# Performance work log

Measured on AMD Instinct MI355X. Metric: run time of the kernel, lower is better.

Reference implementation:

```python
import jax, jax.numpy as jnp
import numpy as np
from jax import lax

RADIUS = 2

def make_kernels(radius):
    # Faithfully reproduces the torch __init__, INCLUDING the bug where
    # NE is computed from the already-normalized NW and SE from SW.
    r = radius
    k = 2 * r + 1
    w = np.ones((k, k), dtype=np.float32)
    L = w.copy(); L[:, r + 1:] = 0
    R = w.copy(); R[:, :r] = 0
    U = w.copy(); U[r + 1:, :] = 0
    D = w.copy(); D[:r, :] = 0
    NW, NE, SW, SE = U.copy(), U.copy(), D.copy(), D.copy()
    half = (r + 1) * k
    L = L / half; R = R / half; U = U / half; D = D / half
    NW[:, r + 1:] = 0
    NE[:, :r] = 0
    SW[:, r + 1:] = 0
    SE[:, :r] = 0
    NW = NW / (r + 1) ** 2
    NE = NW / (r + 1) ** 2  # bug in original: uses new NW
    SW = SW / (r + 1) ** 2
    SE = SW / (r + 1) ** 2  # bug in original: uses new SW
    # order matches d channels 0..7 in forward: L,R,U,D,NW,NE,SW,SE
    return jnp.asarray(np.stack([L, R, U, D, NW, NE, SW, SE])[:, None])  # [8,1,k,k]

def setup_inputs() -> dict:
    key = jax.random.key(0)
    x = jax.random.uniform(key, (8, 3, 768, 768), dtype=jnp.float32)
    return {"x": x, "kernels": make_kernels(RADIUS), "iteration": 3}

def reference(x, kernels, iteration):
    B, C, H, W = x.shape
    k = kernels.shape[-1]
    r = (k - 1) // 2
    # fuse the per-channel loop: treat each (image, channel) as its own sample
    xc = x.reshape(B * C, 1, H, W)

    def step(xc, _):
        # all 8 directional box filters in one conv: [BC,8,H,W]
        conv = lax.conv_general_dilated(
            xc, kernels, window_strides=(1, 1), padding=[(r, r), (r, r)],
            dimension_numbers=("NCHW", "OIHW", "NCHW"))
        d = conv - xc                                   # [BC,8,H,W]
        idx = jnp.argmin(jnp.abs(d), axis=1, keepdims=True)
        dm = jnp.take_along_axis(d, idx, axis=1)        # [BC,1,H,W]
        return xc + dm, None

    xc, _ = lax.scan(step, xc, None, length=iteration)
    return xc.reshape(B, C, H, W)
```

## Files before the change

kernel.cpp:

```cpp
#include <hip/hip_runtime.h>
#include <math.h>


typedef float f4v __attribute__((ext_vector_type(4)));
typedef float f2v __attribute__((ext_vector_type(2), aligned(8)));

#define TW 64
#define TH 32

template<int H2, int W2, bool LAST>
__device__ __forceinline__ void step(const float* __restrict__ X,
                                     float* __restrict__ Y,
                                     float* __restrict__ outp,
                                     int gy0, int gx0, int tid) {
    constexpr int PW = W2 + 4;
    constexpr int SC = W2 / 4;
    constexpr int NSEG = H2 * SC;
    const float w15 = 1.0f / 15.0f;
    const float w9  = 1.0f / 9.0f;
    const float w81 = (1.0f / 9.0f) / 9.0f;

    const bool interior = (gy0 >= 0) && (gx0 >= 0) &&
                          (gy0 + H2 <= 768) && (gx0 + W2 <= 768);

    for (int s = tid; s < NSEG; s += 256) {
        const int y  = s / SC;
        const int xs = (s - y * SC) * 4;
        const float* rp = X + y * PW + xs;

        float acc[8][4];
        #pragma unroll
        for (int d = 0; d < 8; d++)
            #pragma unroll
            for (int j = 0; j < 4; j++) acc[d][j] = 0.0f;
        float ctr[4];

        #pragma unroll
        for (int r = 0; r < 5; r++) {
            const float* p = rp + r * PW;
            f4v lo = *(const f4v*)p;
            f4v hi = *(const f4v*)(p + 4);
            float w[8] = {lo.x, lo.y, lo.z, lo.w, hi.x, hi.y, hi.z, hi.w};

            #pragma unroll
            for (int j = 0; j < 4; j++) {
                acc[0][j] = fmaf(w15, w[j + 0], acc[0][j]);
                acc[0][j] = fmaf(w15, w[j + 1], acc[0][j]);
                acc[0][j] = fmaf(w15, w[j + 2], acc[0][j]);
                acc[1][j] = fmaf(w15, w[j + 2], acc[1][j]);
                acc[1][j] = fmaf(w15, w[j + 3], acc[1][j]);
                acc[1][j] = fmaf(w15, w[j + 4], acc[1][j]);
                if (r < 3) {
                    acc[2][j] = fmaf(w15, w[j + 0], acc[2][j]);
                    acc[2][j] = fmaf(w15, w[j + 1], acc[2][j]);
                    acc[2][j] = fmaf(w15, w[j + 2], acc[2][j]);
                    acc[2][j] = fmaf(w15, w[j + 3], acc[2][j]);
                    acc[2][j] = fmaf(w15, w[j + 4], acc[2][j]);
                    acc[4][j] = fmaf(w9,  w[j + 0], acc[4][j]);
                    acc[4][j] = fmaf(w9,  w[j + 1], acc[4][j]);
                    acc[4][j] = fmaf(w9,  w[j + 2], acc[4][j]);
                    acc[5][j] = fmaf(w81, w[j + 0], acc[5][j]);
                    acc[5][j] = fmaf(w81, w[j + 1], acc[5][j]);
                    acc[5][j] = fmaf(w81, w[j + 2], acc[5][j]);
                }
                if (r >= 2) {
                    acc[3][j] = fmaf(w15, w[j + 0], acc[3][j]);
                    acc[3][j] = fmaf(w15, w[j + 1], acc[3][j]);
                    acc[3][j] = fmaf(w15, w[j + 2], acc[3][j]);
                    acc[3][j] = fmaf(w15, w[j + 3], acc[3][j]);
                    acc[3][j] = fmaf(w15, w[j + 4], acc[3][j]);
                    acc[6][j] = fmaf(w9,  w[j + 0], acc[6][j]);
                    acc[6][j] = fmaf(w9,  w[j + 1], acc[6][j]);
                    acc[6][j] = fmaf(w9,  w[j + 2], acc[6][j]);
                    acc[7][j] = fmaf(w81, w[j + 0], acc[7][j]);
                    acc[7][j] = fmaf(w81, w[j + 1], acc[7][j]);
                    acc[7][j] = fmaf(w81, w[j + 2], acc[7][j]);
                }
                if (r == 2) ctr[j] = w[j + 2];
            }
        }

        f4v R;
        #pragma unroll
        for (int j = 0; j < 4; j++) {
            const float c = ctr[j];
            const float e0 = acc[0][j] - c, e1 = acc[1][j] - c;
            const float e2 = acc[2][j] - c, e3 = acc[3][j] - c;
            const float e4 = acc[4][j] - c, e5 = acc[5][j] - c;
            const float e6 = acc[6][j] - c, e7 = acc[7][j] - c;
            float m01 = (fabsf(e1) < fabsf(e0)) ? e1 : e0;
            float m23 = (fabsf(e3) < fabsf(e2)) ? e3 : e2;
            float m45 = (fabsf(e5) < fabsf(e4)) ? e5 : e4;
            float m67 = (fabsf(e7) < fabsf(e6)) ? e7 : e6;
            float mA  = (fabsf(m23) < fabsf(m01)) ? m23 : m01;
            float mB  = (fabsf(m67) < fabsf(m45)) ? m67 : m45;
            float bd  = (fabsf(mB)  < fabsf(mA))  ? mB  : mA;
            const float res = c + bd;
            if (j == 0) R.x = res; else if (j == 1) R.y = res;
            else if (j == 2) R.z = res; else R.w = res;
        }

        if (LAST) {
            *(f4v*)(outp + y * 768 + xs) = R;
        } else if (interior) {
            *(f4v*)(Y + y * W2 + xs) = R;
        } else {
            const bool rowin = ((unsigned)(gy0 + y) < 768u);
            R.x = (rowin && (unsigned)(gx0 + xs + 0) < 768u) ? R.x : 0.0f;
            R.y = (rowin && (unsigned)(gx0 + xs + 1) < 768u) ? R.y : 0.0f;
            R.z = (rowin && (unsigned)(gx0 + xs + 2) < 768u) ? R.z : 0.0f;
            R.w = (rowin && (unsigned)(gx0 + xs + 3) < 768u) ? R.w : 0.0f;
            *(f4v*)(Y + y * W2 + xs) = R;
        }
    }
    __syncthreads();
}

__global__ __launch_bounds__(256) void swf_fused(const float* __restrict__ in,
                                                 float* __restrict__ out) {
    __shared__ __align__(16) float A[44 * 76];
    __shared__ __align__(16) float B[40 * 72];

    const int tid = threadIdx.x;
    const int tx0 = blockIdx.x * TW;
    const int ty0 = blockIdx.y * TH;
    const long long base = (long long)blockIdx.z * (768 * 768);
    const float* inp = in + base;

    for (int i = tid; i < 44 * 38; i += 256) {
        const int ly  = i / 38;
        const int lx2 = i - ly * 38;
        const int gy  = ty0 + ly - 6;
        const int gx  = tx0 + lx2 * 2 - 6;
        f2v v = {0.0f, 0.0f};
        if ((unsigned)gy < 768u) {
            const float* g = inp + gy * 768 + gx;
            if ((unsigned)gx < 767u) {
                v = *(const f2v*)g;
            } else {
                if ((unsigned)gx < 768u)       v.x = g[0];
                if ((unsigned)(gx + 1) < 768u) v.y = g[1];
            }
        }
        *(f2v*)(A + ly * 76 + lx2 * 2) = v;
    }
    __syncthreads();

    step<40, 72, false>(A, B, nullptr, ty0 - 4, tx0 - 4, tid);
    step<36, 68, false>(B, A, nullptr, ty0 - 2, tx0 - 2, tid);
    step<32, 64, true >(A, nullptr,
                        out + base + (long long)ty0 * 768 + tx0, ty0, tx0, tid);
}

extern "C" void kernel_launch(void* const* d_in, const int* in_sizes, int n_in,
                              void* d_out, int out_size, void* d_ws, size_t ws_size,
                              hipStream_t stream) {
    const float* x = (const float*)d_in[0];
    float* out = (float*)d_out;

    dim3 grid(768 / TW, 768 / TH, 24);
    dim3 block(256);
    swf_fused<<<grid, block, 0, stream>>>(x, out);
}
```

Baseline: 205.6 us.

## Split fused three-iteration kernel into three single-step launches via workspace

Adds a single-iteration kernel that loads only a radius-2 halo tile and computes one filter step, then runs it three times, ping-ponging between the output and workspace buffers. This removes the redundant halo recomputation and the large shared-memory footprint of the fused temporal-blocking kernel, and raises occupancy through smaller LDS and launch bounds of 8. The cost is two extra full-image global round trips and two more kernel launches. The fused kernel remains as a fallback when no workspace is available.

```diff
diff --git a/kernel.cpp b/kernel.cpp
--- a/kernel.cpp
+++ b/kernel.cpp
@@ -7,6 +7,125 @@
 
 #define TW 64
 #define TH 32
+
+template<int PW>
+__device__ __forceinline__ f4v swf4(const float* __restrict__ rp) {
+    const float w15 = 1.0f / 15.0f;
+    const float w9  = 1.0f / 9.0f;
+    const float w81 = (1.0f / 9.0f) / 9.0f;
+
+    float acc[8][4];
+    #pragma unroll
+    for (int d = 0; d < 8; d++)
+        #pragma unroll
+        for (int j = 0; j < 4; j++) acc[d][j] = 0.0f;
+    float ctr[4];
+
+    #pragma unroll
+    for (int r = 0; r < 5; r++) {
+        const float* p = rp + r * PW;
+        f4v lo = *(const f4v*)p;
+        f4v hi = *(const f4v*)(p + 4);
+        float w[8] = {lo.x, lo.y, lo.z, lo.w, hi.x, hi.y, hi.z, hi.w};
+
+        #pragma unroll
+        for (int j = 0; j < 4; j++) {
+            acc[0][j] = fmaf(w15, w[j + 0], acc[0][j]);
+            acc[0][j] = fmaf(w15, w[j + 1], acc[0][j]);
+            acc[0][j] = fmaf(w15, w[j + 2], acc[0][j]);
+            acc[1][j] = fmaf(w15, w[j + 2], acc[1][j]);
+            acc[1][j] = fmaf(w15, w[j + 3], acc[1][j]);
+            acc[1][j] = fmaf(w15, w[j + 4], acc[1][j]);
+            if (r < 3) {
+                acc[2][j] = fmaf(w15, w[j + 0], acc[2][j]);
+                acc[2][j] = fmaf(w15, w[j + 1], acc[2][j]);
+                acc[2][j] = fmaf(w15, w[j + 2], acc[2][j]);
+                acc[2][j] = fmaf(w15, w[j + 3], acc[2][j]);
+                acc[2][j] = fmaf(w15, w[j + 4], acc[2][j]);
+                acc[4][j] = fmaf(w9,  w[j + 0], acc[4][j]);
+                acc[4][j] = fmaf(w9,  w[j + 1], acc[4][j]);
+                acc[4][j] = fmaf(w9,  w[j + 2], acc[4][j]);
+                acc[5][j] = fmaf(w81, w[j + 0], acc[5][j]);
+                acc[5][j] = fmaf(w81, w[j + 1], acc[5][j]);
+                acc[5][j] = fmaf(w81, w[j + 2], acc[5][j]);
+            }
+            if (r >= 2) {
+                acc[3][j] = fmaf(w15, w[j + 0], acc[3][j]);
+                acc[3][j] = fmaf(w15, w[j + 1], acc[3][j]);
+                acc[3][j] = fmaf(w15, w[j + 2], acc[3][j]);
+                acc[3][j] = fmaf(w15, w[j + 3], acc[3][j]);
+                acc[3][j] = fmaf(w15, w[j + 4], acc[3][j]);
+                acc[6][j] = fmaf(w9,  w[j + 0], acc[6][j]);
+                acc[6][j] = fmaf(w9,  w[j + 1], acc[6][j]);
+                acc[6][j] = fmaf(w9,  w[j + 2], acc[6][j]);
+                acc[7][j] = fmaf(w81, w[j + 0], acc[7][j]);
+                acc[7][j] = fmaf(w81, w[j + 1], acc[7][j]);
+                acc[7][j] = fmaf(w81, w[j + 2], acc[7][j]);
+            }
+            if (r == 2) ctr[j] = w[j + 2];
+        }
+    }
+
+    f4v R;
+    #pragma unroll
+    for (int j = 0; j < 4; j++) {
+        const float c = ctr[j];
+        const float e0 = acc[0][j] - c, e1 = acc[1][j] - c;
+        const float e2 = acc[2][j] - c, e3 = acc[3][j] - c;
+        const float e4 = acc[4][j] - c, e5 = acc[5][j] - c;
+        const float e6 = acc[6][j] - c, e7 = acc[7][j] - c;
+        float m01 = (fabsf(e1) < fabsf(e0)) ? e1 : e0;
+        float m23 = (fabsf(e3) < fabsf(e2)) ? e3 : e2;
+        float m45 = (fabsf(e5) < fabsf(e4)) ? e5 : e4;
+        float m67 = (fabsf(e7) < fabsf(e6)) ? e7 : e6;
+        float mA  = (fabsf(m23) < fabsf(m01)) ? m23 : m01;
+        float mB  = (fabsf(m67) < fabsf(m45)) ? m67 : m45;
+        float bd  = (fabsf(mB)  < fabsf(mA))  ? mB  : mA;
+        const float res = c + bd;
+        if (j == 0) R.x = res; else if (j == 1) R.y = res;
+        else if (j == 2) R.z = res; else R.w = res;
+    }
+    return R;
+}
+
+__global__ __launch_bounds__(256, 8) void swf_step1(const float* __restrict__ in,
+                                                    float* __restrict__ out) {
+    __shared__ __align__(16) float A[36 * 68];
+
+    const int tid = threadIdx.x;
+    const int tx0 = blockIdx.x * TW;
+    const int ty0 = blockIdx.y * TH;
+    const long long base = (long long)blockIdx.z * (768 * 768);
+    const float* inp = in + base;
+
+    for (int i = tid; i < 36 * 34; i += 256) {
+        const int ly  = i / 34;
+        const int lx2 = i - ly * 34;
+        const int gy  = ty0 + ly - 2;
+        const int gx  = tx0 + lx2 * 2 - 2;
+        f2v v = {0.0f, 0.0f};
+        if ((unsigned)gy < 768u) {
+            const float* g = inp + gy * 768 + gx;
+            if ((unsigned)gx < 767u) {
+                v = *(const f2v*)g;
+            } else {
+                if ((unsigned)gx < 768u)       v.x = g[0];
+                if ((unsigned)(gx + 1) < 768u) v.y = g[1];
+            }
+        }
+        *(f2v*)(A + ly * 68 + lx2 * 2) = v;
+    }
+    __syncthreads();
+
+    float* op = out + base + (long long)ty0 * 768 + tx0;
+    #pragma unroll 1
+    for (int s = tid; s < 512; s += 256) {
+        const int y  = s >> 4;
+        const int xs = (s & 15) * 4;
+        f4v R = swf4<68>(A + y * 68 + xs);
+        *(f4v*)(op + y * 768 + xs) = R;
+    }
+}
 
 template<int H2, int W2, bool LAST>
 __device__ __forceinline__ void step(const float* __restrict__ X,
@@ -16,9 +135,6 @@
     constexpr int PW = W2 + 4;
     constexpr int SC = W2 / 4;
     constexpr int NSEG = H2 * SC;
-    const float w15 = 1.0f / 15.0f;
-    const float w9  = 1.0f / 9.0f;
-    const float w81 = (1.0f / 9.0f) / 9.0f;
 
     const bool interior = (gy0 >= 0) && (gx0 >= 0) &&
                           (gy0 + H2 <= 768) && (gx0 + W2 <= 768);
@@ -26,79 +142,7 @@
     for (int s = tid; s < NSEG; s += 256) {
         const int y  = s / SC;
         const int xs = (s - y * SC) * 4;
-        const float* rp = X + y * PW + xs;
-
-        float acc[8][4];
-        #pragma unroll
-        for (int d = 0; d < 8; d++)
-            #pragma unroll
-            for (int j = 0; j < 4; j++) acc[d][j] = 0.0f;
-        float ctr[4];
-
-        #pragma unroll
-        for (int r = 0; r < 5; r++) {
-            const float* p = rp + r * PW;
-            f4v lo = *(const f4v*)p;
-            f4v hi = *(const f4v*)(p + 4);
-            float w[8] = {lo.x, lo.y, lo.z, lo.w, hi.x, hi.y, hi.z, hi.w};
-
-            #pragma unroll
-            for (int j = 0; j < 4; j++) {
-                acc[0][j] = fmaf(w15, w[j + 0], acc[0][j]);
-                acc[0][j] = fmaf(w15, w[j + 1], acc[0][j]);
-                acc[0][j] = fmaf(w15, w[j + 2], acc[0][j]);
-                acc[1][j] = fmaf(w15, w[j + 2], acc[1][j]);
-                acc[1][j] = fmaf(w15, w[j + 3], acc[1][j]);
-                acc[1][j] = fmaf(w15, w[j + 4], acc[1][j]);
-                if (r < 3) {
-                    acc[2][j] = fmaf(w15, w[j + 0], acc[2][j]);
-                    acc[2][j] = fmaf(w15, w[j + 1], acc[2][j]);
-                    acc[2][j] = fmaf(w15, w[j + 2], acc[2][j]);
-                    acc[2][j] = fmaf(w15, w[j + 3], acc[2][j]);
-                    acc[2][j] = fmaf(w15, w[j + 4], acc[2][j]);
-                    acc[4][j] = fmaf(w9,  w[j + 0], acc[4][j]);
-                    acc[4][j] = fmaf(w9,  w[j + 1], acc[4][j]);
-                    acc[4][j] = fmaf(w9,  w[j + 2], acc[4][j]);
-                    acc[5][j] = fmaf(w81, w[j + 0], acc[5][j]);
-                    acc[5][j] = fmaf(w81, w[j + 1], acc[5][j]);
-                    acc[5][j] = fmaf(w81, w[j + 2], acc[5][j]);
-                }
-                if (r >= 2) {
-                    acc[3][j] = fmaf(w15, w[j + 0], acc[3][j]);
-                    acc[3][j] = fmaf(w15, w[j + 1], acc[3][j]);
-                    acc[3][j] = fmaf(w15, w[j + 2], acc[3][j]);
-                    acc[3][j] = fmaf(w15, w[j + 3], acc[3][j]);
-                    acc[3][j] = fmaf(w15, w[j + 4], acc[3][j]);
-                    acc[6][j] = fmaf(w9,  w[j + 0], acc[6][j]);
-                    acc[6][j] = fmaf(w9,  w[j + 1], acc[6][j]);
-                    acc[6][j] = fmaf(w9,  w[j + 2], acc[6][j]);
-                    acc[7][j] = fmaf(w81, w[j + 0], acc[7][j]);
-                    acc[7][j] = fmaf(w81, w[j + 1], acc[7][j]);
-                    acc[7][j] = fmaf(w81, w[j + 2], acc[7][j]);
-                }
-                if (r == 2) ctr[j] = w[j + 2];
-            }
-        }
-
-        f4v R;
-        #pragma unroll
-        for (int j = 0; j < 4; j++) {
-            const float c = ctr[j];
-            const float e0 = acc[0][j] - c, e1 = acc[1][j] - c;
-            const float e2 = acc[2][j] - c, e3 = acc[3][j] - c;
-            const float e4 = acc[4][j] - c, e5 = acc[5][j] - c;
-            const float e6 = acc[6][j] - c, e7 = acc[7][j] - c;
-            float m01 = (fabsf(e1) < fabsf(e0)) ? e1 : e0;
-            float m23 = (fabsf(e3) < fabsf(e2)) ? e3 : e2;
-            float m45 = (fabsf(e5) < fabsf(e4)) ? e5 : e4;
-            float m67 = (fabsf(e7) < fabsf(e6)) ? e7 : e6;
-            float mA  = (fabsf(m23) < fabsf(m01)) ? m23 : m01;
-            float mB  = (fabsf(m67) < fabsf(m45)) ? m67 : m45;
-            float bd  = (fabsf(mB)  < fabsf(mA))  ? mB  : mA;
-            const float res = c + bd;
-            if (j == 0) R.x = res; else if (j == 1) R.y = res;
-            else if (j == 2) R.z = res; else R.w = res;
-        }
+        f4v R = swf4<PW>(X + y * PW + xs);
 
         if (LAST) {
             *(f4v*)(outp + y * 768 + xs) = R;
@@ -158,7 +202,16 @@
     const float* x = (const float*)d_in[0];
     float* out = (float*)d_out;
 
+    const size_t IMG_BYTES = (size_t)768 * 768 * 24 * sizeof(float);
     dim3 grid(768 / TW, 768 / TH, 24);
     dim3 block(256);
-    swf_fused<<<grid, block, 0, stream>>>(x, out);
-}
+
+    if (ws_size >= IMG_BYTES && d_ws != nullptr) {
+        float* ws = (float*)d_ws;
+        swf_step1<<<grid, block, 0, stream>>>(x, out);
+        swf_step1<<<grid, block, 0, stream>>>(out, ws);
+        swf_step1<<<grid, block, 0, stream>>>(ws, out);
+    } else {
+        swf_fused<<<grid, block, 0, stream>>>(x, out);
+    }
+}
```

New measurement: 223.0 us. 8.5% more time.

## Reuse vertical partial sums across rows via per-thread row-marching chains

Applied to the files above, without the earlier changes.

Each thread now walks a vertical strip of rows with stride two instead of handling independent 4-pixel segments. The lower-half filters (D, SW, SE) computed for one output row are reused as the upper-half filters (U, NW, NE) for the row two below, and the shared L/R sums are computed once as six 3-tap sums. This removes about half the FMAs per output. In exchange, per-thread work becomes serial along a chain, with fewer threads active per step and possible load imbalance across bands.

```diff
diff --git a/kernel.cpp b/kernel.cpp
--- a/kernel.cpp
+++ b/kernel.cpp
@@ -5,112 +5,153 @@
 typedef float f4v __attribute__((ext_vector_type(4)));
 typedef float f2v __attribute__((ext_vector_type(2), aligned(8)));
 
-#define TW 64
-#define TH 32
-
-template<int H2, int W2, bool LAST>
-__device__ __forceinline__ void step(const float* __restrict__ X,
-                                     float* __restrict__ Y,
-                                     float* __restrict__ outp,
-                                     int gy0, int gx0, int tid) {
-    constexpr int PW = W2 + 4;
-    constexpr int SC = W2 / 4;
-    constexpr int NSEG = H2 * SC;
+template<int PW, bool FULL>
+__device__ __forceinline__ void swf_row(const float* __restrict__ rp,
+        float* Rv, float* Dv, float* SWv, float* SEv,
+        float* Uv, float* NWv, float* NEv, float* ctr) {
     const float w15 = 1.0f / 15.0f;
     const float w9  = 1.0f / 9.0f;
     const float w81 = (1.0f / 9.0f) / 9.0f;
 
+    #pragma unroll
+    for (int r = 0; r < 5; r++) {
+        const float* p = rp + r * PW;
+        f4v lo = *(const f4v*)p;
+        f4v hi = *(const f4v*)(p + 4);
+        float w[8] = {lo.x, lo.y, lo.z, lo.w, hi.x, hi.y, hi.z, hi.w};
+
+        #pragma unroll
+        for (int q = 0; q < 6; q++) {
+            float a = (r == 0) ? (w15 * w[q]) : fmaf(w15, w[q], Rv[q]);
+            a = fmaf(w15, w[q + 1], a);
+            a = fmaf(w15, w[q + 2], a);
+            Rv[q] = a;
+        }
+
+        #pragma unroll
+        for (int j = 0; j < 4; j++) {
+            if (FULL && r < 3) {
+                float u = (r == 0) ? (w15 * w[j]) : fmaf(w15, w[j], Uv[j]);
+                u = fmaf(w15, w[j + 1], u);
+                u = fmaf(w15, w[j + 2], u);
+                u = fmaf(w15, w[j + 3], u);
+                u = fmaf(w15, w[j + 4], u);
+                Uv[j] = u;
+                float nw = (r == 0) ? (w9 * w[j]) : fmaf(w9, w[j], NWv[j]);
+                nw = fmaf(w9, w[j + 1], nw);
+                nw = fmaf(w9, w[j + 2], nw);
+                NWv[j] = nw;
+                float ne = (r == 0) ? (w81 * w[j]) : fmaf(w81, w[j], NEv[j]);
+                ne = fmaf(w81, w[j + 1], ne);
+                ne = fmaf(w81, w[j + 2], ne);
+                NEv[j] = ne;
+            }
+            if (r >= 2) {
+                float d = (r == 2) ? (w15 * w[j]) : fmaf(w15, w[j], Dv[j]);
+                d = fmaf(w15, w[j + 1], d);
+                d = fmaf(w15, w[j + 2], d);
+                d = fmaf(w15, w[j + 3], d);
+                d = fmaf(w15, w[j + 4], d);
+                Dv[j] = d;
+                float sw = (r == 2) ? (w9 * w[j]) : fmaf(w9, w[j], SWv[j]);
+                sw = fmaf(w9, w[j + 1], sw);
+                sw = fmaf(w9, w[j + 2], sw);
+                SWv[j] = sw;
+                float se = (r == 2) ? (w81 * w[j]) : fmaf(w81, w[j], SEv[j]);
+                se = fmaf(w81, w[j + 1], se);
+                se = fmaf(w81, w[j + 2], se);
+                SEv[j] = se;
+                if (r == 2) ctr[j] = w[j + 2];
+            }
+        }
+    }
+}
+
+template<int W2, bool LAST>
+__device__ __forceinline__ void emit_store(const float* Rv,
+        const float* Ua, const float* NWa, const float* NEa,
+        const float* Dn, const float* SWn, const float* SEn, const float* ctr,
+        float* __restrict__ Y, float* __restrict__ outp,
+        int y, int x0, int gy0, int gx0, bool interior) {
+    f4v R;
+    #pragma unroll
+    for (int j = 0; j < 4; j++) {
+        const float c  = ctr[j];
+        const float e0 = Rv[j]     - c;
+        const float e1 = Rv[j + 2] - c;
+        const float e2 = Ua[j]     - c;
+        const float e3 = Dn[j]     - c;
+        const float e4 = NWa[j]    - c;
+        const float e5 = NEa[j]    - c;
+        const float e6 = SWn[j]    - c;
+        const float e7 = SEn[j]    - c;
+        float m01 = (fabsf(e1) < fabsf(e0)) ? e1 : e0;
+        float m23 = (fabsf(e3) < fabsf(e2)) ? e3 : e2;
+        float m45 = (fabsf(e5) < fabsf(e4)) ? e5 : e4;
+        float m67 = (fabsf(e7) < fabsf(e6)) ? e7 : e6;
+        float mA  = (fabsf(m23) < fabsf(m01)) ? m23 : m01;
+        float mB  = (fabsf(m67) < fabsf(m45)) ? m67 : m45;
+        float bd  = (fabsf(mB)  < fabsf(mA))  ? mB  : mA;
+        const float res = c + bd;
+        if (j == 0) R.x = res; else if (j == 1) R.y = res;
+        else if (j == 2) R.z = res; else R.w = res;
+    }
+    if (LAST) {
+        *(f4v*)(outp + y * 768 + x0) = R;
+    } else if (interior) {
+        *(f4v*)(Y + y * W2 + x0) = R;
+    } else {
+        const bool rowin = ((unsigned)(gy0 + y) < 768u);
+        R.x = (rowin && (unsigned)(gx0 + x0 + 0) < 768u) ? R.x : 0.0f;
+        R.y = (rowin && (unsigned)(gx0 + x0 + 1) < 768u) ? R.y : 0.0f;
+        R.z = (rowin && (unsigned)(gx0 + x0 + 2) < 768u) ? R.z : 0.0f;
+        R.w = (rowin && (unsigned)(gx0 + x0 + 3) < 768u) ? R.w : 0.0f;
+        *(f4v*)(Y + y * W2 + x0) = R;
+    }
+}
+
+template<int H2, int W2, bool LAST>
+__device__ __forceinline__ void stepv(const float* __restrict__ X,
+                                      float* __restrict__ Y,
+                                      float* __restrict__ outp,
+                                      int gy0, int gx0, int tid) {
+    constexpr int PW     = W2 + 4;
+    constexpr int STRIPS = W2 / 4;
+    constexpr int BA     = 256 / (2 * STRIPS);
+    constexpr int BH     = (((H2 + BA - 1) / BA) + 1) & ~1;
+    static_assert(BA * BH >= H2, "bands must cover the tile");
+
     const bool interior = (gy0 >= 0) && (gx0 >= 0) &&
                           (gy0 + H2 <= 768) && (gx0 + W2 <= 768);
 
-    for (int s = tid; s < NSEG; s += 256) {
-        const int y  = s / SC;
-        const int xs = (s - y * SC) * 4;
-        const float* rp = X + y * PW + xs;
-
-        float acc[8][4];
-        #pragma unroll
-        for (int d = 0; d < 8; d++)
+    const int chain = tid / STRIPS;
+    const int strip = tid - chain * STRIPS;
+    if (chain < 2 * BA) {
+        const int band = chain >> 1;
+        const int par  = chain & 1;
+        const int x0   = strip * 4;
+        int y = band * BH + par;
+        const int yEnd = (band * BH + BH < H2) ? (band * BH + BH) : H2;
+        if (y < yEnd) {
+            float Rv[6], Dn[4], SWn[4], SEn[4], Uv[4], NWv[4], NEv[4], ctr[4];
+            float pD[4], pSW[4], pSE[4];
+            swf_row<PW, true>(X + y * PW + x0, Rv, Dn, SWn, SEn, Uv, NWv, NEv, ctr);
+            emit_store<W2, LAST>(Rv, Uv, NWv, NEv, Dn, SWn, SEn, ctr,
+                                 Y, outp, y, x0, gy0, gx0, interior);
             #pragma unroll
-            for (int j = 0; j < 4; j++) acc[d][j] = 0.0f;
-        float ctr[4];
-
-        #pragma unroll
-        for (int r = 0; r < 5; r++) {
-            const float* p = rp + r * PW;
-            f4v lo = *(const f4v*)p;
-            f4v hi = *(const f4v*)(p + 4);
-            float w[8] = {lo.x, lo.y, lo.z, lo.w, hi.x, hi.y, hi.z, hi.w};
-
+            for (int j = 0; j < 4; j++) { pD[j] = Dn[j]; pSW[j] = SWn[j]; pSE[j] = SEn[j]; }
             #pragma unroll
-            for (int j = 0; j < 4; j++) {
-                acc[0][j] = fmaf(w15, w[j + 0], acc[0][j]);
-                acc[0][j] = fmaf(w15, w[j + 1], acc[0][j]);
-                acc[0][j] = fmaf(w15, w[j + 2], acc[0][j]);
-                acc[1][j] = fmaf(w15, w[j + 2], acc[1][j]);
-                acc[1][j] = fmaf(w15, w[j + 3], acc[1][j]);
-                acc[1][j] = fmaf(w15, w[j + 4], acc[1][j]);
-                if (r < 3) {
-                    acc[2][j] = fmaf(w15, w[j + 0], acc[2][j]);
-                    acc[2][j] = fmaf(w15, w[j + 1], acc[2][j]);
-                    acc[2][j] = fmaf(w15, w[j + 2], acc[2][j]);
-                    acc[2][j] = fmaf(w15, w[j + 3], acc[2][j]);
-                    acc[2][j] = fmaf(w15, w[j + 4], acc[2][j]);
-                    acc[4][j] = fmaf(w9,  w[j + 0], acc[4][j]);
-                    acc[4][j] = fmaf(w9,  w[j + 1], acc[4][j]);
-                    acc[4][j] = fmaf(w9,  w[j + 2], acc[4][j]);
-                    acc[5][j] = fmaf(w81, w[j + 0], acc[5][j]);
-                    acc[5][j] = fmaf(w81, w[j + 1], acc[5][j]);
-                    acc[5][j] = fmaf(w81, w[j + 2], acc[5][j]);
+            for (int it = 1; it < BH / 2; it++) {
+                y += 2;
+                if (y < yEnd) {
+                    swf_row<PW, false>(X + y * PW + x0, Rv, Dn, SWn, SEn,
+                                       Uv, NWv, NEv, ctr);
+                    emit_store<W2, LAST>(Rv, pD, pSW, pSE, Dn, SWn, SEn, ctr,
+                                         Y, outp, y, x0, gy0, gx0, interior);
+                    #pragma unroll
+                    for (int j = 0; j < 4; j++) { pD[j] = Dn[j]; pSW[j] = SWn[j]; pSE[j] = SEn[j]; }
                 }
-                if (r >= 2) {
-                    acc[3][j] = fmaf(w15, w[j + 0], acc[3][j]);
-                    acc[3][j] = fmaf(w15, w[j + 1], acc[3][j]);
-                    acc[3][j] = fmaf(w15, w[j + 2], acc[3][j]);
-                    acc[3][j] = fmaf(w15, w[j + 3], acc[3][j]);
-                    acc[3][j] = fmaf(w15, w[j + 4], acc[3][j]);
-                    acc[6][j] = fmaf(w9,  w[j + 0], acc[6][j]);
-                    acc[6][j] = fmaf(w9,  w[j + 1], acc[6][j]);
-                    acc[6][j] = fmaf(w9,  w[j + 2], acc[6][j]);
-                    acc[7][j] = fmaf(w81, w[j + 0], acc[7][j]);
-                    acc[7][j] = fmaf(w81, w[j + 1], acc[7][j]);
-                    acc[7][j] = fmaf(w81, w[j + 2], acc[7][j]);
-                }
-                if (r == 2) ctr[j] = w[j + 2];
-            }
-        }
-
-        f4v R;
-        #pragma unroll
-        for (int j = 0; j < 4; j++) {
-            const float c = ctr[j];
-            const float e0 = acc[0][j] - c, e1 = acc[1][j] - c;
-            const float e2 = acc[2][j] - c, e3 = acc[3][j] - c;
-            const float e4 = acc[4][j] - c, e5 = acc[5][j] - c;
-            const float e6 = acc[6][j] - c, e7 = acc[7][j] - c;
-            float m01 = (fabsf(e1) < fabsf(e0)) ? e1 : e0;
-            float m23 = (fabsf(e3) < fabsf(e2)) ? e3 : e2;
-            float m45 = (fabsf(e5) < fabsf(e4)) ? e5 : e4;
-            float m67 = (fabsf(e7) < fabsf(e6)) ? e7 : e6;
-            float mA  = (fabsf(m23) < fabsf(m01)) ? m23 : m01;
-            float mB  = (fabsf(m67) < fabsf(m45)) ? m67 : m45;
-            float bd  = (fabsf(mB)  < fabsf(mA))  ? mB  : mA;
-            const float res = c + bd;
-            if (j == 0) R.x = res; else if (j == 1) R.y = res;
-            else if (j == 2) R.z = res; else R.w = res;
-        }
-
-        if (LAST) {
-            *(f4v*)(outp + y * 768 + xs) = R;
-        } else if (interior) {
-            *(f4v*)(Y + y * W2 + xs) = R;
-        } else {
-            const bool rowin = ((unsigned)(gy0 + y) < 768u);
-            R.x = (rowin && (unsigned)(gx0 + xs + 0) < 768u) ? R.x : 0.0f;
-            R.y = (rowin && (unsigned)(gx0 + xs + 1) < 768u) ? R.y : 0.0f;
-            R.z = (rowin && (unsigned)(gx0 + xs + 2) < 768u) ? R.z : 0.0f;
-            R.w = (rowin && (unsigned)(gx0 + xs + 3) < 768u) ? R.w : 0.0f;
-            *(f4v*)(Y + y * W2 + xs) = R;
+            }
         }
     }
     __syncthreads();
@@ -122,8 +163,8 @@
     __shared__ __align__(16) float B[40 * 72];
 
     const int tid = threadIdx.x;
-    const int tx0 = blockIdx.x * TW;
-    const int ty0 = blockIdx.y * TH;
+    const int tx0 = blockIdx.x * 64;
+    const int ty0 = blockIdx.y * 32;
     const long long base = (long long)blockIdx.z * (768 * 768);
     const float* inp = in + base;
 
@@ -146,10 +187,10 @@
     }
     __syncthreads();
 
-    step<40, 72, false>(A, B, nullptr, ty0 - 4, tx0 - 4, tid);
-    step<36, 68, false>(B, A, nullptr, ty0 - 2, tx0 - 2, tid);
-    step<32, 64, true >(A, nullptr,
-                        out + base + (long long)ty0 * 768 + tx0, ty0, tx0, tid);
+    stepv<40, 72, false>(A, B, nullptr, ty0 - 4, tx0 - 4, tid);
+    stepv<36, 68, false>(B, A, nullptr, ty0 - 2, tx0 - 2, tid);
+    stepv<32, 64, true >(A, nullptr,
+                         out + base + (long long)ty0 * 768 + tx0, ty0, tx0, tid);
 }
 
 extern "C" void kernel_launch(void* const* d_in, const int* in_sizes, int n_in,
@@ -158,7 +199,7 @@
     const float* x = (const float*)d_in[0];
     float* out = (float*)d_out;
 
-    dim3 grid(768 / TW, 768 / TH, 24);
+    dim3 grid(768 / 64, 768 / 32, 24);
     dim3 block(256);
     swf_fused<<<grid, block, 0, stream>>>(x, out);
 }
```

Measured after the change: 195.0 us. 5.2% less time.
